# Kernel optimization log

Hardware: AMD Instinct MI355X
Metric: run time of the kernel (lower is better)

## Reference

```python
import jax, jax.numpy as jnp
import numpy as np

DEPTH, B, S, E, H, EXP = 6, 16, 511, 1024, 16, 2
HD = E // H
FF = EXP * E


def _layernorm(x, g, b, eps=1e-5):
    m = jnp.mean(x, axis=-1, keepdims=True)
    v = jnp.var(x, axis=-1, keepdims=True)
    return (x - m) * jax.lax.rsqrt(v + eps) * g + b


def setup_inputs() -> dict:
    key = jax.random.key(0)
    ks = jax.random.split(key, 12)
    sc = 0.02
    inp = {
        "x": jax.random.normal(ks[0], (B, S, E), jnp.float32),
        "cls_token": jax.random.normal(ks[1], (1, 1, E), jnp.float32),
        "pos_emb": jax.random.normal(ks[2], (1, S + 1, E), jnp.float32),
        # attention projections (bias=False in source), stacked over depth
        "Wq": jax.random.normal(ks[3], (DEPTH, E, E), jnp.float32) * sc,
        "Wk": jax.random.normal(ks[4], (DEPTH, E, E), jnp.float32) * sc,
        "Wv": jax.random.normal(ks[5], (DEPTH, E, E), jnp.float32) * sc,
        "Wp": jax.random.normal(ks[6], (DEPTH, E, E), jnp.float32) * sc,
        # layernorm params
        "ln1_g": jnp.ones((DEPTH, E), jnp.float32),
        "ln1_b": jnp.zeros((DEPTH, E), jnp.float32),
        "ln2_g": jnp.ones((DEPTH, E), jnp.float32),
        "ln2_b": jnp.zeros((DEPTH, E), jnp.float32),
        # feed-forward (with bias, as nn.Linear default)
        "W1": jax.random.normal(ks[7], (DEPTH, E, FF), jnp.float32) * sc,
        "b1": jnp.zeros((DEPTH, FF), jnp.float32),
        "W2": jax.random.normal(ks[8], (DEPTH, FF, E), jnp.float32) * sc,
        "b2": jnp.zeros((DEPTH, E), jnp.float32),
    }
    return inp


def reference(x, cls_token, pos_emb, Wq, Wk, Wv, Wp,
              ln1_g, ln1_b, ln2_g, ln2_b, W1, b1, W2, b2):
    b = x.shape[0]
    # AddClsToken + PositionalEmbedding
    h = jnp.concatenate([jnp.broadcast_to(cls_token, (b, 1, E)), x], axis=1) + pos_emb
    scale = jnp.asarray(E ** 0.5, h.dtype)  # source scales by sqrt(emb_size)
    for i in range(DEPTH):
        # --- self-attention sublayer (pre-LN) ---
        res = h
        xn = _layernorm(h, ln1_g[i], ln1_b[i])
        q = (xn @ Wq[i]).reshape(b, -1, H, HD).transpose(0, 2, 1, 3)  # b h n d
        k = (xn @ Wk[i]).reshape(b, -1, H, HD).transpose(0, 2, 1, 3)
        v = (xn @ Wv[i]).reshape(b, -1, H, HD).transpose(0, 2, 1, 3)
        energy = jnp.einsum('bhqd,bhkd->bhqk', q, k)
        att = jax.nn.softmax(energy / scale, axis=-1)
        out = jnp.einsum('bhqk,bhkd->bhqd', att, v)
        out = out.transpose(0, 2, 1, 3).reshape(b, -1, E)
        h = out @ Wp[i] + res
        # --- feed-forward sublayer (pre-LN) ---
        res = h
        yn = _layernorm(h, ln2_g[i], ln2_b[i])
        ff = jax.nn.gelu(yn @ W1[i] + b1[i], approximate=False) @ W2[i] + b2[i]
        h = ff + res
    return h
```

## Files before the change

kernel.cpp:

```cpp
#include <hip/hip_runtime.h>
#include <cstdint>
#include <cstddef>

#define DEPTH 6
#define NB    16
#define NSEQ  512
#define EMB   1024
#define NHEAD 16
#define HDIM  64
#define FFD   2048
#define NTOK  (NB * NSEQ)

typedef unsigned short u16;
using bf16x8 = __attribute__((ext_vector_type(8))) __bf16;
using f32x4  = __attribute__((ext_vector_type(4))) float;
using u16x4  = __attribute__((ext_vector_type(4))) u16;

typedef __attribute__((address_space(1))) uint32_t* as1_u32p;
typedef __attribute__((address_space(3))) uint32_t* as3_u32p;
typedef __attribute__((address_space(3))) u16*      as3_u16p;

__device__ __forceinline__ u16 f2bf(float f) {
  union { float f; uint32_t u; } v; v.f = f;
  uint32_t u = v.u;
  return (u16)((u + 0x7FFFu + ((u >> 16) & 1u)) >> 16);
}

__device__ __forceinline__ void gload_lds16(const u16* g, u16* l) {
  void* gp = const_cast<u16*>(g);
  __builtin_amdgcn_global_load_lds((as1_u32p)gp, (as3_u32p)l, 16, 0, 0);
}

template<int ROWBYTES>
__device__ __forceinline__ void stage16k(const u16* g0, int ldk, u16* lds) {
  int t = threadIdx.x;
#pragma unroll
  for (int i = 0; i < 4; ++i) {
    int off = (i * 256 + t) * 16;
    int row = off / ROWBYTES;
    int pc  = (off % ROWBYTES) >> 4;
    int lc  = pc ^ (row & 7);
    gload_lds16(g0 + (size_t)row * ldk + lc * 8, lds + (off >> 1));
  }
}

__global__ __launch_bounds__(256)
void wprep_k(const float* __restrict__ W, u16* __restrict__ Wt,
             int K, int N, size_t inL, size_t outL, size_t outOff)
{
  int ntiles = N >> 6, ktiles = K >> 6;
  int bid = blockIdx.x;
  int l = bid / (ktiles * ntiles);
  int r = bid % (ktiles * ntiles);
  int kt = r / ntiles, nt = r % ntiles;
  const float* in = W + (size_t)l * inL + (size_t)(kt * 64) * N + nt * 64;
  u16* out = Wt + (size_t)l * outL + outOff + (size_t)(nt * 64) * K + kt * 64;
  __shared__ float tile[64][65];
  int t = threadIdx.x;
  int tr = t >> 4, tc = (t & 15) * 4;
#pragma unroll
  for (int i = 0; i < 4; ++i) {
    f32x4 v = *(const f32x4*)(in + (size_t)(tr + i * 16) * N + tc);
    tile[tr + i * 16][tc + 0] = v[0];
    tile[tr + i * 16][tc + 1] = v[1];
    tile[tr + i * 16][tc + 2] = v[2];
    tile[tr + i * 16][tc + 3] = v[3];
  }
  __syncthreads();
#pragma unroll
  for (int i = 0; i < 4; ++i) {
    int nr = tr + i * 16;
    u16x4 o;
    o[0] = f2bf(tile[tc + 0][nr]);
    o[1] = f2bf(tile[tc + 1][nr]);
    o[2] = f2bf(tile[tc + 2][nr]);
    o[3] = f2bf(tile[tc + 3][nr]);
    *(u16x4*)(out + (size_t)nr * K + tc) = o;
  }
}

__global__ __launch_bounds__(256)
void embed_k(const float* __restrict__ x, const float* __restrict__ cls,
             const float* __restrict__ pos, float* __restrict__ H)
{
  int row = blockIdx.x, t = threadIdx.x;
  int b_ = row >> 9, n = row & 511;
  int c = t * 4;
  f32x4 p = *(const f32x4*)(pos + (size_t)n * EMB + c);
  f32x4 s;
  if (n == 0) s = *(const f32x4*)(cls + c);
  else        s = *(const f32x4*)(x + ((size_t)b_ * 511 + (n - 1)) * EMB + c);
  f32x4 o = s + p;
  *(f32x4*)(H + (size_t)row * EMB + c) = o;
}

__global__ __launch_bounds__(256)
void ln_k(const float* __restrict__ H, const float* __restrict__ g,
          const float* __restrict__ b, u16* __restrict__ out)
{
  int row = blockIdx.x, t = threadIdx.x;
  const float* hp = H + (size_t)row * EMB;
  f32x4 v = *(const f32x4*)(hp + t * 4);
  float s  = v[0] + v[1] + v[2] + v[3];
  float ss = v[0]*v[0] + v[1]*v[1] + v[2]*v[2] + v[3]*v[3];
#pragma unroll
  for (int m = 1; m <= 32; m <<= 1) { s += __shfl_xor(s, m); ss += __shfl_xor(ss, m); }
  __shared__ float red[8];
  if ((t & 63) == 0) { red[(t >> 6) * 2] = s; red[(t >> 6) * 2 + 1] = ss; }
  __syncthreads();
  float S  = red[0] + red[2] + red[4] + red[6];
  float SS = red[1] + red[3] + red[5] + red[7];
  float mean = S * (1.0f / EMB);
  float var  = SS * (1.0f / EMB) - mean * mean;
  float rs = rsqrtf(var + 1e-5f);
  f32x4 gg = *(const f32x4*)(g + t * 4);
  f32x4 bb = *(const f32x4*)(b + t * 4);
  u16x4 o;
#pragma unroll
  for (int i = 0; i < 4; ++i) o[i] = f2bf((v[i] - mean) * rs * gg[i] + bb[i]);
  *(u16x4*)(out + (size_t)row * EMB + t * 4) = o;
}

template<int EPI>
__global__ __launch_bounds__(256, 2)
void gemm_k(const u16* __restrict__ A, const u16* __restrict__ Bt,
            int nbn, int K,
            const float* __restrict__ bias, float* __restrict__ H,
            u16* __restrict__ outB,
            u16* __restrict__ qo, u16* __restrict__ ko, u16* __restrict__ vto)
{
  __shared__ u16 sm[2][2][128 * 64];
  int cpx = gridDim.x >> 3;
  int logical = (blockIdx.x & 7) * cpx + (blockIdx.x >> 3);
  int bm = logical / nbn, bn = logical % nbn;
  int t = threadIdx.x, lane = t & 63, w = t >> 6;
  int wm = w >> 1, wn = w & 1;
  const u16* Ab = A  + (size_t)(bm * 128) * K;
  const u16* Bb = Bt + (size_t)(bn * 128) * K;
  int nkt = K >> 6;

  stage16k<128>(Ab, K, &sm[0][0][0]);
  stage16k<128>(Bb, K, &sm[0][1][0]);
  __syncthreads();

  const f32x4 vzero = {0.f, 0.f, 0.f, 0.f};
  f32x4 acc[4][4];
#pragma unroll
  for (int i = 0; i < 4; ++i)
#pragma unroll
    for (int j = 0; j < 4; ++j) acc[i][j] = vzero;

  int r0 = lane & 15;
  int kk0 = (lane >> 4) * 8;

  for (int kt = 0; kt < nkt; ++kt) {
    int cur = kt & 1;
    if (kt + 1 < nkt) {
      stage16k<128>(Ab + (kt + 1) * 64, K, &sm[cur ^ 1][0][0]);
      stage16k<128>(Bb + (kt + 1) * 64, K, &sm[cur ^ 1][1][0]);
    }
    const char* smA = (const char*)&sm[cur][0][0];
    const char* smB = (const char*)&sm[cur][1][0];
#pragma unroll
    for (int ks = 0; ks < 2; ++ks) {
      int kk = ks * 32 + kk0;
      bf16x8 a[4], b[4];
#pragma unroll
      for (int mf = 0; mf < 4; ++mf) {
        int row = wm * 64 + mf * 16 + r0;
        a[mf] = *(const bf16x8*)(smA + row * 128 + ((kk * 2) ^ ((row & 7) << 4)));
      }
#pragma unroll
      for (int nf = 0; nf < 4; ++nf) {
        int row = wn * 64 + nf * 16 + r0;
        b[nf] = *(const bf16x8*)(smB + row * 128 + ((kk * 2) ^ ((row & 7) << 4)));
      }
#pragma unroll
      for (int mf = 0; mf < 4; ++mf)
#pragma unroll
        for (int nf = 0; nf < 4; ++nf)
          acc[mf][nf] = __builtin_amdgcn_mfma_f32_16x16x32_bf16(a[mf], b[nf], acc[mf][nf], 0, 0, 0);
    }
    __syncthreads();
  }

  int m0 = bm * 128 + wm * 64;
  int n0 = bn * 128 + wn * 64;
  int hi = lane >> 4;
#pragma unroll
  for (int mf = 0; mf < 4; ++mf) {
#pragma unroll
    for (int nf = 0; nf < 4; ++nf) {
      int col  = n0 + nf * 16 + r0;
      int rowb = m0 + mf * 16 + hi * 4;
      if (EPI == 0) {
        int which = col >> 10, c = col & 1023;
        int hh = c >> 6, d = c & 63;
        int b_ = rowb >> 9, n_ = rowb & 511;
        size_t bh = (size_t)(b_ * NHEAD + hh);
        if (which == 2) {
          u16x4 o;
#pragma unroll
          for (int j = 0; j < 4; ++j) o[j] = f2bf(acc[mf][nf][j]);
          *(u16x4*)(vto + (bh * HDIM + d) * NSEQ + n_) = o;
        } else {
          u16* dst = (which == 0) ? qo : ko;
#pragma unroll
          for (int j = 0; j < 4; ++j)
            dst[(bh * NSEQ + n_ + j) * HDIM + d] = f2bf(acc[mf][nf][j]);
        }
      } else {
#pragma unroll
        for (int j = 0; j < 4; ++j) {
          int row = rowb + j;
          float v = acc[mf][nf][j];
          if (EPI == 1) {
            size_t idx = (size_t)row * EMB + col;
            H[idx] = v + H[idx];
          } else if (EPI == 2) {
            float xg = v + bias[col];
            float ge = 0.5f * xg * (1.0f + erff(xg * 0.70710678118654752f));
            outB[(size_t)row * FFD + col] = f2bf(ge);
          } else {
            size_t idx = (size_t)row * EMB + col;
            H[idx] = v + bias[col] + H[idx];
          }
        }
      }
    }
  }
}

__global__ __launch_bounds__(256, 3)
void attn_k(const u16* __restrict__ Q, const u16* __restrict__ Kk,
            const u16* __restrict__ Vt, u16* __restrict__ AO)
{
  __shared__ u16 kv[2][8192];
  __shared__ u16 Pt[4][2048];
  int bid = blockIdx.x;
  int bh = (bid & 7) * 32 + (bid >> 6);
  int qt = (bid >> 3) & 7;
  int t = threadIdx.x, lane = t & 63, w = t >> 6;
  const u16* Kb = Kk + (size_t)bh * (NSEQ * HDIM);
  const u16* Vb = Vt + (size_t)bh * (HDIM * NSEQ);
  int r0 = lane & 15, hi = lane >> 4, kk0 = hi * 8;

  int qrow = qt * 64 + w * 16 + r0;
  const u16* Qp = Q + ((size_t)bh * NSEQ + qrow) * HDIM;
  bf16x8 qf0 = *(const bf16x8*)(Qp + kk0);
  bf16x8 qf1 = *(const bf16x8*)(Qp + 32 + kk0);

  const f32x4 vzero = {0.f, 0.f, 0.f, 0.f};
  f32x4 accS[32];
#pragma unroll
  for (int f = 0; f < 32; ++f) accS[f] = vzero;

  stage16k<128>(Kb, HDIM, &kv[0][0]);
  __syncthreads();
#pragma unroll
  for (int kt = 0; kt < 4; ++kt) {
    if (kt < 3) stage16k<128>(Kb + (size_t)(kt + 1) * 128 * HDIM, HDIM, &kv[(kt + 1) & 1][0]);
    const char* smK = (const char*)&kv[kt & 1][0];
#pragma unroll
    for (int nfl = 0; nfl < 8; ++nfl) {
      int krow = nfl * 16 + r0;
      int swz = (krow & 7) << 4;
      bf16x8 b0 = *(const bf16x8*)(smK + krow * 128 + (((kk0)      * 2) ^ swz));
      bf16x8 b1 = *(const bf16x8*)(smK + krow * 128 + (((32 + kk0) * 2) ^ swz));
      accS[kt * 8 + nfl] = __builtin_amdgcn_mfma_f32_16x16x32_bf16(qf0, b0, accS[kt * 8 + nfl], 0, 0, 0);
      accS[kt * 8 + nfl] = __builtin_amdgcn_mfma_f32_16x16x32_bf16(qf1, b1, accS[kt * 8 + nfl], 0, 0, 0);
    }
    __syncthreads();
  }

  stage16k<256>(Vb, NSEQ, &kv[0][0]);

  float mx[4], den[4], rden[4];
#pragma unroll
  for (int j = 0; j < 4; ++j) {
    float m = -1e30f;
#pragma unroll
    for (int f = 0; f < 32; ++f) m = fmaxf(m, accS[f][j]);
    m = fmaxf(m, __shfl_xor(m, 1));
    m = fmaxf(m, __shfl_xor(m, 2));
    m = fmaxf(m, __shfl_xor(m, 4));
    m = fmaxf(m, __shfl_xor(m, 8));
    mx[j] = m;
    den[j] = 0.f;
  }
  uint32_t pb[64];
#pragma unroll
  for (int f = 0; f < 32; ++f) {
    float p0 = __expf((accS[f][0] - mx[0]) * 0.03125f);
    float p1 = __expf((accS[f][1] - mx[1]) * 0.03125f);
    float p2 = __expf((accS[f][2] - mx[2]) * 0.03125f);
    float p3 = __expf((accS[f][3] - mx[3]) * 0.03125f);
    den[0] += p0; den[1] += p1; den[2] += p2; den[3] += p3;
    pb[f * 2 + 0] = (uint32_t)f2bf(p0) | ((uint32_t)f2bf(p1) << 16);
    pb[f * 2 + 1] = (uint32_t)f2bf(p2) | ((uint32_t)f2bf(p3) << 16);
  }
#pragma unroll
  for (int j = 0; j < 4; ++j) {
    float d = den[j];
    d += __shfl_xor(d, 1); d += __shfl_xor(d, 2);
    d += __shfl_xor(d, 4); d += __shfl_xor(d, 8);
    rden[j] = 1.0f / d;
  }
  __syncthreads();

  int perm0 = ((r0 & 4) << 2) + ((r0 >> 3) << 2) + (r0 & 3);
  uint32_t ptb = (uint32_t)(uintptr_t)(as3_u16p)&Pt[w][0];
  uint32_t trBase = ptb + r0 * 2 + hi * 128;
  char* PtW = (char*)&Pt[w][0];

  f32x4 accO[4];
#pragma unroll
  for (int nf = 0; nf < 4; ++nf) accO[nf] = vzero;

#pragma unroll
  for (int kt = 0; kt < 4; ++kt) {
    if (kt < 3) stage16k<256>(Vb + (kt + 1) * 128, NSEQ, &kv[(kt + 1) & 1][0]);
#pragma unroll
    for (int fl = 0; fl < 8; ++fl) {
      int f = kt * 8 + fl;
      int row = (fl >> 1) * 32 + perm0 + ((fl & 1) << 3);
      *(uint2*)(PtW + row * 32 + hi * 8) = make_uint2(pb[f * 2], pb[f * 2 + 1]);
    }
    asm volatile("s_waitcnt lgkmcnt(0)" ::: "memory");
    const char* smV = (const char*)&kv[kt & 1][0];
#pragma unroll
    for (int s = 0; s < 4; ++s) {
      uint2 t0, t1;
      uint32_t a0 = trBase + s * 1024;
      asm volatile("ds_read_b64_tr_b16 %0, %1" : "=v"(t0) : "v"(a0) : "memory");
      asm volatile("ds_read_b64_tr_b16 %0, %1" : "=v"(t1) : "v"(a0 + 512) : "memory");
      bf16x8 vb[4];
#pragma unroll
      for (int nf = 0; nf < 4; ++nf) {
        int d = nf * 16 + r0;
        int inrow = s * 64 + hi * 16;
        vb[nf] = *(const bf16x8*)(smV + d * 256 + (inrow ^ ((d & 7) << 4)));
      }
      asm volatile("s_waitcnt lgkmcnt(0)" ::: "memory");
      __builtin_amdgcn_sched_barrier(0);
      union { uint4 u; bf16x8 v; } pa;
      pa.u = make_uint4(t0.x, t0.y, t1.x, t1.y);
#pragma unroll
      for (int nf = 0; nf < 4; ++nf)
        accO[nf] = __builtin_amdgcn_mfma_f32_16x16x32_bf16(pa.v, vb[nf], accO[nf], 0, 0, 0);
    }
    __syncthreads();
  }

  int b_ = bh >> 4, hh = bh & 15;
#pragma unroll
  for (int nf = 0; nf < 4; ++nf)
#pragma unroll
    for (int j = 0; j < 4; ++j) {
      int ql = hi * 4 + j;
      int tok = qt * 64 + w * 16 + ql;
      int col = hh * 64 + nf * 16 + r0;
      AO[((size_t)(b_ * NSEQ + tok)) * EMB + col] = f2bf(accO[nf][j] * rden[j]);
    }
}

extern "C" void kernel_launch(void* const* d_in, const int* in_sizes, int n_in,
                              void* d_out, int out_size, void* d_ws, size_t ws_size,
                              hipStream_t stream)
{
  const float* x    = (const float*)d_in[0];
  const float* cls  = (const float*)d_in[1];
  const float* pos  = (const float*)d_in[2];
  const float* Wq   = (const float*)d_in[3];
  const float* Wk   = (const float*)d_in[4];
  const float* Wv   = (const float*)d_in[5];
  const float* Wp   = (const float*)d_in[6];
  const float* ln1g = (const float*)d_in[7];
  const float* ln1b = (const float*)d_in[8];
  const float* ln2g = (const float*)d_in[9];
  const float* ln2b = (const float*)d_in[10];
  const float* W1   = (const float*)d_in[11];
  const float* b1   = (const float*)d_in[12];
  const float* W2   = (const float*)d_in[13];
  const float* b2   = (const float*)d_in[14];
  float* H = (float*)d_out;

  char* ws = (char*)d_ws;
  u16* wqkv = (u16*)(ws + 0);
  u16* wp   = (u16*)(ws + 37748736);
  u16* w1t  = (u16*)(ws + 50331648);
  u16* w2t  = (u16*)(ws + 75497472);
  u16* xn   = (u16*)(ws + 100663296);
  u16* qb   = (u16*)(ws + 117440512);
  u16* kb   = (u16*)(ws + 134217728);
  u16* vtb  = (u16*)(ws + 150994944);
  u16* ffb  = qb;

  wprep_k<<<1536, 256, 0, stream>>>(Wq, wqkv, 1024, 1024, 1048576, 3145728, 0);
  wprep_k<<<1536, 256, 0, stream>>>(Wk, wqkv, 1024, 1024, 1048576, 3145728, 1048576);
  wprep_k<<<1536, 256, 0, stream>>>(Wv, wqkv, 1024, 1024, 1048576, 3145728, 2097152);
  wprep_k<<<1536, 256, 0, stream>>>(Wp, wp,   1024, 1024, 1048576, 1048576, 0);
  wprep_k<<<3072, 256, 0, stream>>>(W1, w1t,  1024, 2048, 2097152, 2097152, 0);
  wprep_k<<<3072, 256, 0, stream>>>(W2, w2t,  2048, 1024, 2097152, 2097152, 0);

  embed_k<<<NTOK, 256, 0, stream>>>(x, cls, pos, H);

  for (int l = 0; l < DEPTH; ++l) {
    ln_k<<<NTOK, 256, 0, stream>>>(H, ln1g + l * EMB, ln1b + l * EMB, xn);
    gemm_k<0><<<64 * 24, 256, 0, stream>>>(xn, wqkv + (size_t)l * 3145728, 24, 1024,
                                           nullptr, nullptr, nullptr, qb, kb, vtb);
    attn_k<<<2048, 256, 0, stream>>>(qb, kb, vtb, xn);
    gemm_k<1><<<64 * 8, 256, 0, stream>>>(xn, wp + (size_t)l * 1048576, 8, 1024,
                                          nullptr, H, nullptr, nullptr, nullptr, nullptr);
    ln_k<<<NTOK, 256, 0, stream>>>(H, ln2g + l * EMB, ln2b + l * EMB, xn);
    gemm_k<2><<<64 * 16, 256, 0, stream>>>(xn, w1t + (size_t)l * 2097152, 16, 1024,
                                           b1 + l * FFD, nullptr, ffb, nullptr, nullptr, nullptr);
    gemm_k<3><<<64 * 8, 256, 0, stream>>>(ffb, w2t + (size_t)l * 2097152, 8, 2048,
                                          b2 + l * EMB, H, nullptr, nullptr, nullptr, nullptr);
  }
}
```

Measured before the change: 1.555 ms.

## Add 256x256-tile 8-wave GEMM with ping-pong LDS schedule for QKV and FF1

Adds a 512-thread GEMM kernel with 256x256 output tiles for the QKV projection and the first feed-forward GEMM. It splits the A and B tiles into halves and interleaves global-to-LDS staging, barriers, explicit waitcnt and MFMA priority raises across four sub-tiles per K step. The goal is more data reuse per loaded byte and better overlap of loads with matrix math. In exchange it uses more registers per thread, produces fewer blocks (384 and 256) across the CUs, and relies on hand-tuned vmcnt counts that must match the issued loads.

```diff
diff --git a/kernel.cpp b/kernel.cpp
--- a/kernel.cpp
+++ b/kernel.cpp
@@ -121,13 +121,175 @@
   *(u16x4*)(out + (size_t)row * EMB + t * 4) = o;
 }
 
+
+__device__ __forceinline__ void stageA256(u16* dst, const u16* src, int K,
+                                          int half, int t) {
+#pragma unroll
+  for (int i = 0; i < 2; ++i) {
+    int off = (i * 512 + t) * 16;
+    int chunk = off >> 13;
+    int row_in = (off >> 7) & 63;
+    int lc = ((off >> 4) & 7) ^ (row_in & 7);
+    int grow = chunk * 128 + half * 64 + row_in;
+    gload_lds16(src + (size_t)grow * K + lc * 8, dst + (off >> 1));
+  }
+}
+
+__device__ __forceinline__ void stageB256(u16* dst, const u16* src, int K,
+                                          int half, int t) {
+#pragma unroll
+  for (int i = 0; i < 2; ++i) {
+    int off = (i * 512 + t) * 16;
+    int blk = off >> 12;
+    int row_in = (off >> 7) & 31;
+    int lc = ((off >> 4) & 7) ^ (row_in & 7);
+    int nrow = blk * 64 + half * 32 + row_in;
+    gload_lds16(src + (size_t)nrow * K + lc * 8, dst + (off >> 1));
+  }
+}
+
+#define DS_A(BUF, MH) do {                                                   \
+  const char* _ba = (const char*)&smA[BUF][MH][wm][0];                       \
+  _Pragma("unroll") for (int mf = 0; mf < 4; ++mf) {                         \
+    int ri = mf * 16 + r0; int swz = (r0 & 7) << 4;                          \
+    af[mf][0] = *(const bf16x8*)(_ba + ri * 128 + ((kk0 * 2) ^ swz));        \
+    af[mf][1] = *(const bf16x8*)(_ba + ri * 128 + (((32 + kk0) * 2) ^ swz)); \
+  } } while (0)
+
+#define DS_B(BUF, NH) do {                                                   \
+  const char* _bb = (const char*)&smB[BUF][NH][wn][0];                       \
+  _Pragma("unroll") for (int nf = 0; nf < 2; ++nf) {                         \
+    int ri = nf * 16 + r0; int swz = (r0 & 7) << 4;                          \
+    bfr[nf][0] = *(const bf16x8*)(_bb + ri * 128 + ((kk0 * 2) ^ swz));       \
+    bfr[nf][1] = *(const bf16x8*)(_bb + ri * 128 + (((32 + kk0) * 2) ^ swz));\
+  } } while (0)
+
+#define MFMA16(MH, NH) do {                                                  \
+  __builtin_amdgcn_s_setprio(1);                                             \
+  _Pragma("unroll") for (int ks = 0; ks < 2; ++ks)                           \
+  _Pragma("unroll") for (int mf = 0; mf < 4; ++mf)                           \
+  _Pragma("unroll") for (int nf = 0; nf < 2; ++nf)                           \
+    acc[MH * 4 + mf][NH * 2 + nf] = __builtin_amdgcn_mfma_f32_16x16x32_bf16( \
+        af[mf][ks], bfr[nf][ks], acc[MH * 4 + mf][NH * 2 + nf], 0, 0, 0);    \
+  __builtin_amdgcn_s_setprio(0);                                             \
+} while (0)
+
+#define BAR()       __builtin_amdgcn_s_barrier()
+#define WAIT_LGKM0() do { asm volatile("s_waitcnt lgkmcnt(0)" ::: "memory"); \
+                          __builtin_amdgcn_sched_barrier(0); } while (0)
+#define VMCNT4()    asm volatile("s_waitcnt vmcnt(4)" ::: "memory")
+
+template<int EPI>
+__global__ __launch_bounds__(512, 2)
+void gemm256_k(const u16* __restrict__ A, const u16* __restrict__ Bt,
+               int nbn, int K,
+               const float* __restrict__ bias, u16* __restrict__ outB,
+               u16* __restrict__ qo, u16* __restrict__ ko, u16* __restrict__ vto)
+{
+  __shared__ u16 smA[2][2][2][4096];
+  __shared__ u16 smB[2][2][4][2048];
+
+  int cpx = gridDim.x >> 3;
+  int logical = (blockIdx.x & 7) * cpx + (blockIdx.x >> 3);
+  int bm = logical / nbn, bn = logical % nbn;
+  int t = threadIdx.x, lane = t & 63, w = t >> 6;
+  int wm = w >> 2, wn = w & 3;
+  int r0 = lane & 15, hi = lane >> 4, kk0 = hi * 8;
+  const u16* Ab = A  + (size_t)(bm * 256) * K;
+  const u16* Bb = Bt + (size_t)(bn * 256) * K;
+  int nkt = K >> 6, T = nkt >> 1;
+
+  stageA256(&smA[0][0][0][0], Ab, K, 0, t);
+  stageA256(&smA[0][1][0][0], Ab, K, 1, t);
+  stageB256(&smB[0][0][0][0], Bb, K, 0, t);
+  stageB256(&smB[0][1][0][0], Bb, K, 1, t);
+  stageA256(&smA[1][0][0][0], Ab + 64, K, 0, t);
+  stageB256(&smB[1][1][0][0], Bb + 64, K, 1, t);
+  VMCNT4();
+  BAR();
+
+  const f32x4 vzero = {0.f, 0.f, 0.f, 0.f};
+  f32x4 acc[8][4];
+#pragma unroll
+  for (int i = 0; i < 8; ++i)
+#pragma unroll
+    for (int j = 0; j < 4; ++j) acc[i][j] = vzero;
+
+  bf16x8 af[4][2], bfr[2][2];
+
+  for (int it = 0; it < T; ++it) {
+    int k1 = 2 * it + 1;
+    int k2 = 2 * it + 2; if (k2 > nkt - 1) k2 = nkt - 1;
+    int k3 = 2 * it + 3; if (k3 > nkt - 1) k3 = nkt - 1;
+    DS_A(0, 0); DS_B(0, 0);
+    stageA256(&smA[1][1][0][0], Ab + k1 * 64, K, 1, t);
+    BAR(); WAIT_LGKM0(); MFMA16(0, 0); BAR();
+    DS_B(0, 1);
+    stageB256(&smB[1][0][0][0], Bb + k1 * 64, K, 0, t);
+    BAR(); WAIT_LGKM0(); MFMA16(0, 1); BAR();
+    DS_A(0, 1);
+    stageA256(&smA[0][0][0][0], Ab + k2 * 64, K, 0, t);
+    BAR(); WAIT_LGKM0(); MFMA16(1, 1); BAR();
+    DS_B(0, 0);
+    stageB256(&smB[0][1][0][0], Bb + k2 * 64, K, 1, t);
+    VMCNT4();
+    BAR(); WAIT_LGKM0(); MFMA16(1, 0); BAR();
+    DS_A(1, 0); DS_B(1, 0);
+    stageA256(&smA[0][1][0][0], Ab + k2 * 64, K, 1, t);
+    BAR(); WAIT_LGKM0(); MFMA16(0, 0); BAR();
+    DS_B(1, 1);
+    stageB256(&smB[0][0][0][0], Bb + k2 * 64, K, 0, t);
+    BAR(); WAIT_LGKM0(); MFMA16(0, 1); BAR();
+    DS_A(1, 1);
+    stageA256(&smA[1][0][0][0], Ab + k3 * 64, K, 0, t);
+    BAR(); WAIT_LGKM0(); MFMA16(1, 1); BAR();
+    DS_B(1, 0);
+    stageB256(&smB[1][1][0][0], Bb + k3 * 64, K, 1, t);
+    VMCNT4();
+    BAR(); WAIT_LGKM0(); MFMA16(1, 0); BAR();
+  }
+
+  int m0 = bm * 256 + wm * 128;
+  int n0 = bn * 256 + wn * 64;
+#pragma unroll
+  for (int mi = 0; mi < 8; ++mi) {
+#pragma unroll
+    for (int ni = 0; ni < 4; ++ni) {
+      int col  = n0 + ni * 16 + r0;
+      int rowb = m0 + mi * 16 + hi * 4;
+      if (EPI == 0) {
+        int which = col >> 10, c = col & 1023;
+        int hh = c >> 6, d = c & 63;
+        int b_ = rowb >> 9, n_ = rowb & 511;
+        size_t bh = (size_t)(b_ * NHEAD + hh);
+        if (which == 2) {
+          u16x4 o;
+#pragma unroll
+          for (int j = 0; j < 4; ++j) o[j] = f2bf(acc[mi][ni][j]);
+          *(u16x4*)(vto + (bh * HDIM + d) * NSEQ + n_) = o;
+        } else {
+          u16* dst = (which == 0) ? qo : ko;
+#pragma unroll
+          for (int j = 0; j < 4; ++j)
+            dst[(bh * NSEQ + n_ + j) * HDIM + d] = f2bf(acc[mi][ni][j]);
+        }
+      } else {
+#pragma unroll
+        for (int j = 0; j < 4; ++j) {
+          float xg = acc[mi][ni][j] + bias[col];
+          float ge = 0.5f * xg * (1.0f + erff(xg * 0.70710678118654752f));
+          outB[(size_t)(rowb + j) * FFD + col] = f2bf(ge);
+        }
+      }
+    }
+  }
+}
+
 template<int EPI>
 __global__ __launch_bounds__(256, 2)
 void gemm_k(const u16* __restrict__ A, const u16* __restrict__ Bt,
             int nbn, int K,
-            const float* __restrict__ bias, float* __restrict__ H,
-            u16* __restrict__ outB,
-            u16* __restrict__ qo, u16* __restrict__ ko, u16* __restrict__ vto)
+            const float* __restrict__ bias, float* __restrict__ H)
 {
   __shared__ u16 sm[2][2][128 * 64];
   int cpx = gridDim.x >> 3;
@@ -159,8 +321,8 @@
       stage16k<128>(Ab + (kt + 1) * 64, K, &sm[cur ^ 1][0][0]);
       stage16k<128>(Bb + (kt + 1) * 64, K, &sm[cur ^ 1][1][0]);
     }
-    const char* smA = (const char*)&sm[cur][0][0];
-    const char* smB = (const char*)&sm[cur][1][0];
+    const char* smAp = (const char*)&sm[cur][0][0];
+    const char* smBp = (const char*)&sm[cur][1][0];
 #pragma unroll
     for (int ks = 0; ks < 2; ++ks) {
       int kk = ks * 32 + kk0;
@@ -168,12 +330,12 @@
 #pragma unroll
       for (int mf = 0; mf < 4; ++mf) {
         int row = wm * 64 + mf * 16 + r0;
-        a[mf] = *(const bf16x8*)(smA + row * 128 + ((kk * 2) ^ ((row & 7) << 4)));
+        a[mf] = *(const bf16x8*)(smAp + row * 128 + ((kk * 2) ^ ((row & 7) << 4)));
       }
 #pragma unroll
       for (int nf = 0; nf < 4; ++nf) {
         int row = wn * 64 + nf * 16 + r0;
-        b[nf] = *(const bf16x8*)(smB + row * 128 + ((kk * 2) ^ ((row & 7) << 4)));
+        b[nf] = *(const bf16x8*)(smBp + row * 128 + ((kk * 2) ^ ((row & 7) << 4)));
       }
 #pragma unroll
       for (int mf = 0; mf < 4; ++mf)
@@ -193,39 +355,13 @@
     for (int nf = 0; nf < 4; ++nf) {
       int col  = n0 + nf * 16 + r0;
       int rowb = m0 + mf * 16 + hi * 4;
-      if (EPI == 0) {
-        int which = col >> 10, c = col & 1023;
-        int hh = c >> 6, d = c & 63;
-        int b_ = rowb >> 9, n_ = rowb & 511;
-        size_t bh = (size_t)(b_ * NHEAD + hh);
-        if (which == 2) {
-          u16x4 o;
-#pragma unroll
-          for (int j = 0; j < 4; ++j) o[j] = f2bf(acc[mf][nf][j]);
-          *(u16x4*)(vto + (bh * HDIM + d) * NSEQ + n_) = o;
-        } else {
-          u16* dst = (which == 0) ? qo : ko;
-#pragma unroll
-          for (int j = 0; j < 4; ++j)
-            dst[(bh * NSEQ + n_ + j) * HDIM + d] = f2bf(acc[mf][nf][j]);
-        }
-      } else {
-#pragma unroll
-        for (int j = 0; j < 4; ++j) {
-          int row = rowb + j;
-          float v = acc[mf][nf][j];
-          if (EPI == 1) {
-            size_t idx = (size_t)row * EMB + col;
-            H[idx] = v + H[idx];
-          } else if (EPI == 2) {
-            float xg = v + bias[col];
-            float ge = 0.5f * xg * (1.0f + erff(xg * 0.70710678118654752f));
-            outB[(size_t)row * FFD + col] = f2bf(ge);
-          } else {
-            size_t idx = (size_t)row * EMB + col;
-            H[idx] = v + bias[col] + H[idx];
-          }
-        }
+#pragma unroll
+      for (int j = 0; j < 4; ++j) {
+        int row = rowb + j;
+        float v = acc[mf][nf][j];
+        size_t idx = (size_t)row * EMB + col;
+        if (EPI == 1) H[idx] = v + H[idx];
+        else          H[idx] = v + bias[col] + H[idx];
       }
     }
   }
@@ -407,15 +543,15 @@
 
   for (int l = 0; l < DEPTH; ++l) {
     ln_k<<<NTOK, 256, 0, stream>>>(H, ln1g + l * EMB, ln1b + l * EMB, xn);
-    gemm_k<0><<<64 * 24, 256, 0, stream>>>(xn, wqkv + (size_t)l * 3145728, 24, 1024,
-                                           nullptr, nullptr, nullptr, qb, kb, vtb);
+    gemm256_k<0><<<384, 512, 0, stream>>>(xn, wqkv + (size_t)l * 3145728, 12, 1024,
+                                          nullptr, nullptr, qb, kb, vtb);
     attn_k<<<2048, 256, 0, stream>>>(qb, kb, vtb, xn);
-    gemm_k<1><<<64 * 8, 256, 0, stream>>>(xn, wp + (size_t)l * 1048576, 8, 1024,
-                                          nullptr, H, nullptr, nullptr, nullptr, nullptr);
+    gemm_k<1><<<512, 256, 0, stream>>>(xn, wp + (size_t)l * 1048576, 8, 1024,
+                                       nullptr, H);
     ln_k<<<NTOK, 256, 0, stream>>>(H, ln2g + l * EMB, ln2b + l * EMB, xn);
-    gemm_k<2><<<64 * 16, 256, 0, stream>>>(xn, w1t + (size_t)l * 2097152, 16, 1024,
-                                           b1 + l * FFD, nullptr, ffb, nullptr, nullptr, nullptr);
-    gemm_k<3><<<64 * 8, 256, 0, stream>>>(ffb, w2t + (size_t)l * 2097152, 8, 2048,
-                                          b2 + l * EMB, H, nullptr, nullptr, nullptr, nullptr);
-  }
-}
+    gemm256_k<2><<<256, 512, 0, stream>>>(xn, w1t + (size_t)l * 2097152, 8, 1024,
+                                          b1 + l * FFD, ffb, nullptr, nullptr, nullptr);
+    gemm_k<3><<<512, 256, 0, stream>>>(ffb, w2t + (size_t)l * 2097152, 8, 2048,
+                                       b2 + l * EMB, H);
+  }
+}
```

Measured after the change: 1.613 ms. +3.8%, slower.

## Stage bf16 GEMM epilogue through swizzled LDS for 16-byte stores, single-buffer mainloop

Applied to the files above, without the earlier changes.

The bf16-output GEMM epilogues (QKV scatter and bias+GELU) now write results into a swizzled shared tile, then store coalesced 8-element vectors to global memory, including a transposed path for V. This targets the scattered 2-byte stores of the old epilogue. To make room for more blocks per CU, the mainloop drops double buffering in favour of a single 32 KB LDS tile with a sync after each stage, and the launch bounds rise to 3 blocks per SM. This loses the overlap between global loads and MFMA work within a block, relying on the extra resident blocks to hide it.

```diff
diff --git a/kernel.cpp b/kernel.cpp
--- a/kernel.cpp
+++ b/kernel.cpp
@@ -15,6 +15,7 @@
 using bf16x8 = __attribute__((ext_vector_type(8))) __bf16;
 using f32x4  = __attribute__((ext_vector_type(4))) float;
 using u16x4  = __attribute__((ext_vector_type(4))) u16;
+using u16x8  = __attribute__((ext_vector_type(8))) u16;
 
 typedef __attribute__((address_space(1))) uint32_t* as1_u32p;
 typedef __attribute__((address_space(3))) uint32_t* as3_u32p;
@@ -122,14 +123,14 @@
 }
 
 template<int EPI>
-__global__ __launch_bounds__(256, 2)
+__global__ __launch_bounds__(256, 3)
 void gemm_k(const u16* __restrict__ A, const u16* __restrict__ Bt,
             int nbn, int K,
             const float* __restrict__ bias, float* __restrict__ H,
             u16* __restrict__ outB,
             u16* __restrict__ qo, u16* __restrict__ ko, u16* __restrict__ vto)
 {
-  __shared__ u16 sm[2][2][128 * 64];
+  __shared__ u16 sm[16384];
   int cpx = gridDim.x >> 3;
   int logical = (blockIdx.x & 7) * cpx + (blockIdx.x >> 3);
   int bm = logical / nbn, bn = logical % nbn;
@@ -139,10 +140,6 @@
   const u16* Bb = Bt + (size_t)(bn * 128) * K;
   int nkt = K >> 6;
 
-  stage16k<128>(Ab, K, &sm[0][0][0]);
-  stage16k<128>(Bb, K, &sm[0][1][0]);
-  __syncthreads();
-
   const f32x4 vzero = {0.f, 0.f, 0.f, 0.f};
   f32x4 acc[4][4];
 #pragma unroll
@@ -151,16 +148,15 @@
     for (int j = 0; j < 4; ++j) acc[i][j] = vzero;
 
   int r0 = lane & 15;
-  int kk0 = (lane >> 4) * 8;
+  int hi = lane >> 4;
+  int kk0 = hi * 8;
 
   for (int kt = 0; kt < nkt; ++kt) {
-    int cur = kt & 1;
-    if (kt + 1 < nkt) {
-      stage16k<128>(Ab + (kt + 1) * 64, K, &sm[cur ^ 1][0][0]);
-      stage16k<128>(Bb + (kt + 1) * 64, K, &sm[cur ^ 1][1][0]);
-    }
-    const char* smA = (const char*)&sm[cur][0][0];
-    const char* smB = (const char*)&sm[cur][1][0];
+    stage16k<128>(Ab + kt * 64, K, sm);
+    stage16k<128>(Bb + kt * 64, K, sm + 8192);
+    __syncthreads();
+    const char* smAp = (const char*)sm;
+    const char* smBp = (const char*)(sm + 8192);
 #pragma unroll
     for (int ks = 0; ks < 2; ++ks) {
       int kk = ks * 32 + kk0;
@@ -168,12 +164,12 @@
 #pragma unroll
       for (int mf = 0; mf < 4; ++mf) {
         int row = wm * 64 + mf * 16 + r0;
-        a[mf] = *(const bf16x8*)(smA + row * 128 + ((kk * 2) ^ ((row & 7) << 4)));
+        a[mf] = *(const bf16x8*)(smAp + row * 128 + ((kk * 2) ^ ((row & 7) << 4)));
       }
 #pragma unroll
       for (int nf = 0; nf < 4; ++nf) {
         int row = wn * 64 + nf * 16 + r0;
-        b[nf] = *(const bf16x8*)(smB + row * 128 + ((kk * 2) ^ ((row & 7) << 4)));
+        b[nf] = *(const bf16x8*)(smBp + row * 128 + ((kk * 2) ^ ((row & 7) << 4)));
       }
 #pragma unroll
       for (int mf = 0; mf < 4; ++mf)
@@ -184,49 +180,82 @@
     __syncthreads();
   }
 
-  int m0 = bm * 128 + wm * 64;
-  int n0 = bn * 128 + wn * 64;
-  int hi = lane >> 4;
+  if (EPI == 1 || EPI == 3) {
+    int m0 = bm * 128 + wm * 64;
+    int n0 = bn * 128 + wn * 64;
+#pragma unroll
+    for (int mf = 0; mf < 4; ++mf) {
+#pragma unroll
+      for (int nf = 0; nf < 4; ++nf) {
+        int col  = n0 + nf * 16 + r0;
+        int rowb = m0 + mf * 16 + hi * 4;
+#pragma unroll
+        for (int j = 0; j < 4; ++j) {
+          float v = acc[mf][nf][j];
+          size_t idx = (size_t)(rowb + j) * EMB + col;
+          if (EPI == 1) H[idx] = v + H[idx];
+          else          H[idx] = v + bias[col] + H[idx];
+        }
+      }
+    }
+    return;
+  }
+
+  int sec = (bn * 128) >> 10;
+  bool vsec = (EPI == 0) && (sec == 2);
 #pragma unroll
   for (int mf = 0; mf < 4; ++mf) {
 #pragma unroll
     for (int nf = 0; nf < 4; ++nf) {
-      int col  = n0 + nf * 16 + r0;
-      int rowb = m0 + mf * 16 + hi * 4;
-      if (EPI == 0) {
-        int which = col >> 10, c = col & 1023;
-        int hh = c >> 6, d = c & 63;
-        int b_ = rowb >> 9, n_ = rowb & 511;
-        size_t bh = (size_t)(b_ * NHEAD + hh);
-        if (which == 2) {
-          u16x4 o;
-#pragma unroll
-          for (int j = 0; j < 4; ++j) o[j] = f2bf(acc[mf][nf][j]);
-          *(u16x4*)(vto + (bh * HDIM + d) * NSEQ + n_) = o;
-        } else {
-          u16* dst = (which == 0) ? qo : ko;
-#pragma unroll
-          for (int j = 0; j < 4; ++j)
-            dst[(bh * NSEQ + n_ + j) * HDIM + d] = f2bf(acc[mf][nf][j]);
+      int colL = wn * 64 + nf * 16 + r0;
+#pragma unroll
+      for (int j = 0; j < 4; ++j) {
+        int rowL = wm * 64 + mf * 16 + hi * 4 + j;
+        float v = acc[mf][nf][j];
+        if (EPI == 2) {
+          float xg = v + bias[bn * 128 + colL];
+          v = 0.5f * xg * (1.0f + erff(xg * 0.70710678118654752f));
         }
+        u16 o = f2bf(v);
+        if (!vsec)
+          sm[rowL * 128 + (colL & 7) + ((((colL >> 3) ^ (rowL & 7))) << 3)] = o;
+        else
+          sm[colL * 128 + (rowL & 7) + ((((rowL >> 3) ^ (colL & 7))) << 3)] = o;
+      }
+    }
+  }
+  __syncthreads();
+
+  int c  = t & 15;
+  int rb = t >> 4;
+  if (!vsec) {
+#pragma unroll
+    for (int i = 0; i < 8; ++i) {
+      int row = rb * 8 + i;
+      u16x8 v = *(const u16x8*)(sm + row * 128 + ((c ^ (row & 7)) << 3));
+      if (EPI == 2) {
+        int rowg = bm * 128 + row;
+        int colg = bn * 128 + c * 8;
+        *(u16x8*)(outB + (size_t)rowg * FFD + colg) = v;
       } else {
-#pragma unroll
-        for (int j = 0; j < 4; ++j) {
-          int row = rowb + j;
-          float v = acc[mf][nf][j];
-          if (EPI == 1) {
-            size_t idx = (size_t)row * EMB + col;
-            H[idx] = v + H[idx];
-          } else if (EPI == 2) {
-            float xg = v + bias[col];
-            float ge = 0.5f * xg * (1.0f + erff(xg * 0.70710678118654752f));
-            outB[(size_t)row * FFD + col] = f2bf(ge);
-          } else {
-            size_t idx = (size_t)row * EMB + col;
-            H[idx] = v + bias[col] + H[idx];
-          }
-        }
-      }
+        int n_ = bm * 128 + row;
+        int b_ = n_ >> 9, tok = n_ & 511;
+        int c0 = (bn * 128 - sec * 1024) + c * 8;
+        int hh = c0 >> 6, d0 = c0 & 63;
+        u16* dst = (sec == 0) ? qo : ko;
+        *(u16x8*)(dst + (((size_t)(b_ * NHEAD + hh) * NSEQ + tok) * HDIM) + d0) = v;
+      }
+    }
+  } else {
+#pragma unroll
+    for (int i = 0; i < 8; ++i) {
+      int rowp = rb * 8 + i;
+      u16x8 v = *(const u16x8*)(sm + rowp * 128 + ((c ^ (rowp & 7)) << 3));
+      int c0 = (bn * 128 - 2048) + rowp;
+      int hh = c0 >> 6, d = c0 & 63;
+      int tok0 = bm * 128 + c * 8;
+      int b_ = tok0 >> 9;
+      *(u16x8*)(vto + ((size_t)(b_ * NHEAD + hh) * HDIM + d) * NSEQ + (tok0 & 511)) = v;
     }
   }
 }
```

Result: no change. 1.531 ms (-1.5%).
